# Optimization experiments

Hardware: AMD Instinct MI355X
Metric: run time of the kernel (lower is better)

Reference implementation:

```python
import jax, jax.numpy as jnp
import numpy as np

N_NODES = 50000
N_EDGES = 800000
IN_DIM = 128
E_FEATS = 64
H = 8
D = IN_DIM // H
NEG_SLOPE = 0.2


def setup_inputs() -> dict:
    key = jax.random.key(0)
    ks = jax.random.split(key, 9)
    h = jax.random.normal(ks[0], (N_NODES, IN_DIM), dtype=jnp.float32)
    edge_features = jax.random.normal(ks[1], (N_EDGES, E_FEATS), dtype=jnp.float32)
    src = jax.random.randint(ks[2], (N_EDGES,), 0, N_NODES, dtype=jnp.int32)
    dst = jax.random.randint(ks[3], (N_EDGES,), 0, N_NODES, dtype=jnp.int32)
    s = 0.05
    Wq = jax.random.normal(ks[4], (IN_DIM, IN_DIM), dtype=jnp.float32) * s
    Wk = jax.random.normal(ks[5], (IN_DIM, IN_DIM), dtype=jnp.float32) * s
    Wv = jax.random.normal(ks[6], (IN_DIM, IN_DIM), dtype=jnp.float32) * s
    We = jax.random.normal(ks[7], (H, E_FEATS), dtype=jnp.float32) * s
    Wres = jax.random.normal(ks[8], (IN_DIM, IN_DIM), dtype=jnp.float32) * s
    return {"h": h, "edge_features": edge_features, "src": src, "dst": dst,
            "Wq": Wq, "Wk": Wk, "Wv": Wv, "We": We, "Wres": Wres}


def reference(h, edge_features, src, dst, Wq, Wk, Wv, We, Wres):
    N = h.shape[0]
    # QKV projections (feat_drop is identity at eval)
    q = (h @ Wq.T).reshape(N, H, D)
    k = (h @ Wk.T).reshape(N, H, D)
    v = (h @ Wv.T).reshape(N, H, D)
    # ee / m_att are computed in the original forward but never used (dead code)
    _ee = edge_features @ We.T  # [E, H]

    # v_dot_u('q','k'): dot(q[dst], k[src]) per edge, per head -> [E, H]
    e = jnp.einsum('ehd,ehd->eh', q[dst], k[src])
    e = jnp.where(e >= 0, e, NEG_SLOPE * e)  # leaky_relu

    # edge_softmax over incoming edges of each destination node
    m = jax.ops.segment_max(e, dst, num_segments=N)          # [N, H]
    ex = jnp.exp(e - m[dst])                                 # [E, H]
    z = jax.ops.segment_sum(ex, dst, num_segments=N)         # [N, H]
    alpha = ex / z[dst]                                      # [E, H] (attn_drop identity)

    # weighted aggregation: sum_e alpha * v[src]
    msg = v[src] * alpha[:, :, None]                         # [E, H, D]
    rst = jax.ops.segment_sum(msg, dst, num_segments=N)      # [N, H, D]
    rst = rst.reshape(N, H * D)
    rst = rst + h @ Wres.T                                   # residual
    return rst
```

## Files before the change

### kernel.cpp

```cpp
#include <hip/hip_runtime.h>


#define NEG_SLOPE 0.2f
#define CB 1024

typedef __attribute__((ext_vector_type(8))) short short8;
typedef __attribute__((ext_vector_type(4))) float f32x4;

__device__ __forceinline__ unsigned short f2bf(float f) {
    unsigned int u = __builtin_bit_cast(unsigned int, f);
    u = (u + 0x7fffu + ((u >> 16) & 1u)) >> 16;
    return (unsigned short)u;
}
__device__ __forceinline__ float bf2f(unsigned short s) {
    unsigned int u = (unsigned int)s << 16;
    return __builtin_bit_cast(float, u);
}

__global__ __launch_bounds__(256) void zero_wconv_kernel(
    const float* __restrict__ Wq, const float* __restrict__ Wk,
    const float* __restrict__ Wv, const float* __restrict__ Wres,
    unsigned short* __restrict__ wpk, int* __restrict__ cnt, int n4)
{
    int t = blockIdx.x * 256 + threadIdx.x;
    if (t < 8192) {
        int l = t & 63;
        int v = t >> 6;
        int kk = v & 3;
        int wct = v >> 2;
        int ct = wct & 7;
        int w = wct >> 3;
        const float* W = (w == 0) ? Wq : (w == 1) ? Wk : (w == 2) ? Wv : Wres;
        const float* srcp = W + (size_t)(ct * 16 + (l & 15)) * 128 + kk * 32 + (l >> 4) * 8;
        float4 lo = *reinterpret_cast<const float4*>(srcp);
        float4 hi = *reinterpret_cast<const float4*>(srcp + 4);
        short8 o;
        o[0] = (short)f2bf(lo.x); o[1] = (short)f2bf(lo.y);
        o[2] = (short)f2bf(lo.z); o[3] = (short)f2bf(lo.w);
        o[4] = (short)f2bf(hi.x); o[5] = (short)f2bf(hi.y);
        o[6] = (short)f2bf(hi.z); o[7] = (short)f2bf(hi.w);
        *reinterpret_cast<short8*>(wpk + (size_t)t * 8) = o;
    } else {
        int u = t - 8192;
        if (u < n4) reinterpret_cast<int4*>(cnt)[u] = make_int4(0, 0, 0, 0);
    }
}

__global__ __launch_bounds__(256) void proj_count_kernel(
    const float* __restrict__ h,
    const unsigned short* __restrict__ wpk,
    unsigned short* __restrict__ qb, unsigned short* __restrict__ kvb,
    float* __restrict__ res,
    const int* __restrict__ dst, int* __restrict__ cnt,
    int N, int E, int PB)
{
    if (blockIdx.x >= PB) {
        int start = (blockIdx.x - PB) * 256 + threadIdx.x;
        for (int e = start; e < E; e += CB * 256)
            atomicAdd(&cnt[dst[e]], 1);
        return;
    }

    const int wid = threadIdx.x >> 6;
    const int lane = threadIdx.x & 63;
    const int row0 = blockIdx.x * 128 + wid * 32;
    const int r = lane & 15, g = lane >> 4;

    short8 afrag[2][4];
    #pragma unroll
    for (int grp = 0; grp < 2; ++grp) {
        int arow = row0 + grp * 16 + r;
        if (arow >= N) arow = N - 1;
        const float* hrow = h + (size_t)arow * 128 + g * 8;
        #pragma unroll
        for (int kk = 0; kk < 4; ++kk) {
            float4 lo = *reinterpret_cast<const float4*>(hrow + kk * 32);
            float4 hi = *reinterpret_cast<const float4*>(hrow + kk * 32 + 4);
            short8 a;
            a[0] = (short)f2bf(lo.x); a[1] = (short)f2bf(lo.y);
            a[2] = (short)f2bf(lo.z); a[3] = (short)f2bf(lo.w);
            a[4] = (short)f2bf(hi.x); a[5] = (short)f2bf(hi.y);
            a[6] = (short)f2bf(hi.z); a[7] = (short)f2bf(hi.w);
            afrag[grp][kk] = a;
        }
    }

    for (int w = 0; w < 4; ++w) {
        f32x4 acc[2][8];
        #pragma unroll
        for (int grp = 0; grp < 2; ++grp)
            #pragma unroll
            for (int ct = 0; ct < 8; ++ct) acc[grp][ct] = (f32x4)(0.f);

        #pragma unroll
        for (int ct = 0; ct < 8; ++ct) {
            const unsigned short* bp =
                wpk + ((size_t)((w * 8 + ct) * 4) * 64 + lane) * 8;
            short8 bfrag[4];
            #pragma unroll
            for (int kk = 0; kk < 4; ++kk)
                bfrag[kk] = *reinterpret_cast<const short8*>(bp + (size_t)kk * 512);
            #pragma unroll
            for (int grp = 0; grp < 2; ++grp)
                #pragma unroll
                for (int kk = 0; kk < 4; ++kk)
                    acc[grp][ct] = __builtin_amdgcn_mfma_f32_16x16x32_bf16(
                        afrag[grp][kk], bfrag[kk], acc[grp][ct], 0, 0, 0);
        }

        #pragma unroll
        for (int grp = 0; grp < 2; ++grp) {
            #pragma unroll
            for (int j = 0; j < 4; ++j) {
                int orow = row0 + grp * 16 + g * 4 + j;
                if (orow < N) {
                    if (w == 0) {
                        #pragma unroll
                        for (int ct = 0; ct < 8; ++ct)
                            qb[(size_t)orow * 128 + ct * 16 + r] = f2bf(acc[grp][ct][j]);
                    } else if (w == 3) {
                        #pragma unroll
                        for (int ct = 0; ct < 8; ++ct)
                            res[(size_t)orow * 128 + ct * 16 + r] = acc[grp][ct][j];
                    } else {
                        const int voff = (w == 2) ? 1 : 0;
                        #pragma unroll
                        for (int ct = 0; ct < 8; ++ct) {
                            int idx = ct * 32 + 2 * r + voff;
                            kvb[(size_t)orow * 256 + idx] = f2bf(acc[grp][ct][j]);
                        }
                    }
                }
            }
        }
    }
}

__global__ __launch_bounds__(256) void blocksum_kernel(
    const int* __restrict__ cnt, int* __restrict__ bsum, int N)
{
    __shared__ int ws[4];
    const int tid = threadIdx.x;
    int base = blockIdx.x * 1024 + tid * 4;
    int s = 0;
    if (base + 3 < N) {
        int4 v = *reinterpret_cast<const int4*>(cnt + base);
        s = v.x + v.y + v.z + v.w;
    } else {
        for (int i = 0; i < 4; ++i)
            if (base + i < N) s += cnt[base + i];
    }
    #pragma unroll
    for (int m = 32; m >= 1; m >>= 1) s += __shfl_xor(s, m, 64);
    if ((tid & 63) == 0) ws[tid >> 6] = s;
    __syncthreads();
    if (tid == 0) bsum[blockIdx.x] = ws[0] + ws[1] + ws[2] + ws[3];
}

__global__ __launch_bounds__(256) void scanfinal_kernel(
    const int* __restrict__ cnt, const int* __restrict__ bsum,
    int* __restrict__ row_start, int* __restrict__ cursor,
    int N, int E, int NB)
{
    __shared__ int sboff;
    __shared__ int wsum[4];
    const int tid = threadIdx.x, lane = tid & 63, w = tid >> 6;

    if (tid < 64) {
        int v = (tid < NB && tid < blockIdx.x) ? bsum[tid] : 0;
        #pragma unroll
        for (int m = 32; m >= 1; m >>= 1) v += __shfl_xor(v, m, 64);
        if (tid == 0) sboff = v;
    }
    __syncthreads();

    int base = blockIdx.x * 1024 + tid * 4;
    int a0 = 0, a1 = 0, a2 = 0, a3 = 0;
    if (base + 3 < N) {
        int4 v = *reinterpret_cast<const int4*>(cnt + base);
        a0 = v.x; a1 = v.y; a2 = v.z; a3 = v.w;
    } else {
        if (base + 0 < N) a0 = cnt[base + 0];
        if (base + 1 < N) a1 = cnt[base + 1];
        if (base + 2 < N) a2 = cnt[base + 2];
        if (base + 3 < N) a3 = cnt[base + 3];
    }
    const int tsum = a0 + a1 + a2 + a3;
    int v = tsum;
    #pragma unroll
    for (int off = 1; off < 64; off <<= 1) {
        int t = __shfl_up(v, off, 64);
        if (lane >= off) v += t;
    }
    if (lane == 63) wsum[w] = v;
    __syncthreads();
    int woff = 0;
    for (int i = 0; i < w; ++i) woff += wsum[i];
    int run = sboff + woff + v - tsum;

    int r0 = run, r1 = run + a0, r2 = r1 + a1, r3 = r2 + a2;
    if (base + 3 < N) {
        int4 o = make_int4(r0, r1, r2, r3);
        *reinterpret_cast<int4*>(row_start + base) = o;
        *reinterpret_cast<int4*>(cursor + base) = o;
    } else {
        int rr[4] = {r0, r1, r2, r3};
        for (int i = 0; i < 4; ++i)
            if (base + i < N) { row_start[base + i] = rr[i]; cursor[base + i] = rr[i]; }
    }
    if (blockIdx.x == 0 && tid == 0) row_start[N] = E;
}

__global__ __launch_bounds__(256) void scatter_kernel(
    const int* __restrict__ src, const int* __restrict__ dst,
    int* __restrict__ cursor, int* __restrict__ csr_src, int E)
{
    int e = blockIdx.x * 256 + threadIdx.x;
    if (e < E) {
        int d = dst[e];
        int pos = atomicAdd(&cursor[d], 1);
        csr_src[pos] = src[e];
    }
}

__global__ __launch_bounds__(256) void fused_agg_kernel(
    const unsigned short* __restrict__ qb,
    const unsigned short* __restrict__ kvb,
    const int* __restrict__ row_start, const int* __restrict__ csr_src,
    float* __restrict__ rst, int N)
{
    const int lane = threadIdx.x & 63;
    const int j = lane & 31;
    const int half = lane >> 5;
    const int node = blockIdx.x * 4 + (threadIdx.x >> 6);
    if (node >= N) return;

    const int beg = row_start[node];
    const int nE  = row_start[node + 1] - beg;
    if (nE <= 0) return;
    const int* cp = csr_src + beg;
    const int last = nE - 1;

    ushort4 qraw = *reinterpret_cast<const ushort4*>(qb + (size_t)node * 128 + 4 * j);
    const float q0 = bf2f(qraw.x), q1 = bf2f(qraw.y),
                q2 = bf2f(qraw.z), q3 = bf2f(qraw.w);

    float a0 = 0.f, a1 = 0.f, a2 = 0.f, a3 = 0.f, z = 0.f;

    int sa = cp[min(half, last)];
    int sb = cp[min(half + 2, last)];

    #pragma unroll 2
    for (int i = 0; i < nE; i += 2) {
        const int ii = i + half;
        const float m = (ii < nE) ? 1.f : 0.f;
        const int scur = sa;
        sa = sb;
        sb = cp[min(ii + 4, last)];

        const unsigned short* kp = kvb + (size_t)scur * 256 + 8 * j;
        short8 kv8 = *reinterpret_cast<const short8*>(kp);
        float p = q0 * bf2f((unsigned short)kv8[0])
                + q1 * bf2f((unsigned short)kv8[2])
                + q2 * bf2f((unsigned short)kv8[4])
                + q3 * bf2f((unsigned short)kv8[6]);
        p += __shfl_xor(p, 1, 64);
        p += __shfl_xor(p, 2, 64);
        float e = (p >= 0.f) ? p : NEG_SLOPE * p;
        e = m * __expf(e);
        z += e;
        a0 = fmaf(e, bf2f((unsigned short)kv8[1]), a0);
        a1 = fmaf(e, bf2f((unsigned short)kv8[3]), a1);
        a2 = fmaf(e, bf2f((unsigned short)kv8[5]), a2);
        a3 = fmaf(e, bf2f((unsigned short)kv8[7]), a3);
    }

    a0 += __shfl_xor(a0, 32, 64);
    a1 += __shfl_xor(a1, 32, 64);
    a2 += __shfl_xor(a2, 32, 64);
    a3 += __shfl_xor(a3, 32, 64);
    z  += __shfl_xor(z, 32, 64);

    if (half == 0) {
        const size_t base = (size_t)node * 128 + 4 * j;
        float inv = 1.f / z;
        float4 rv = *reinterpret_cast<const float4*>(rst + base);
        rv.x = fmaf(a0, inv, rv.x);
        rv.y = fmaf(a1, inv, rv.y);
        rv.z = fmaf(a2, inv, rv.z);
        rv.w = fmaf(a3, inv, rv.w);
        *reinterpret_cast<float4*>(rst + base) = rv;
    }
}

extern "C" void kernel_launch(void* const* d_in, const int* in_sizes, int n_in,
                              void* d_out, int out_size, void* d_ws, size_t ws_size,
                              hipStream_t stream) {
    const float* h    = (const float*)d_in[0];
    const int*   src  = (const int*)d_in[2];
    const int*   dst  = (const int*)d_in[3];
    const float* Wq   = (const float*)d_in[4];
    const float* Wk   = (const float*)d_in[5];
    const float* Wv   = (const float*)d_in[6];
    const float* Wres = (const float*)d_in[8];
    float* rst = (float*)d_out;

    const int N = in_sizes[0] / 128;
    const int E = in_sizes[2];

    unsigned short* qb  = (unsigned short*)d_ws;
    unsigned short* kvb = qb + (size_t)N * 128;
    unsigned short* wpk = kvb + (size_t)N * 256;
    int* cnt       = (int*)(wpk + 4 * 16384);
    int* row_start = cnt + N;
    int* cursor    = row_start + (N + 1);
    int* csr_src   = cursor + N;
    int* bsum      = csr_src + E;

    const int n4 = N / 4;
    const int NB = (N + 1023) / 1024;
    const int PB = (N + 127) / 128;

    zero_wconv_kernel<<<(8192 + n4 + 255) / 256, 256, 0, stream>>>(
        Wq, Wk, Wv, Wres, wpk, cnt, n4);
    proj_count_kernel<<<PB + CB, 256, 0, stream>>>(h, wpk, qb, kvb, rst,
                                                   dst, cnt, N, E, PB);
    blocksum_kernel<<<NB, 256, 0, stream>>>(cnt, bsum, N);
    scanfinal_kernel<<<NB, 256, 0, stream>>>(cnt, bsum, row_start, cursor,
                                             N, E, NB);
    scatter_kernel<<<(E + 255) / 256, 256, 0, stream>>>(src, dst, cursor,
                                                        csr_src, E);
    fused_agg_kernel<<<(N + 3) / 4, 256, 0, stream>>>(qb, kvb, row_start,
                                                      csr_src, rst, N);
}
```

Before: 173.8 us.

## Store residual in bf16, pack K/V stores, and unroll aggregation with dual accumulators

The projection kernel now writes the residual projection as bf16 to a workspace buffer instead of fp32 into the output. K and V are computed together per column tile and stored as packed 32-bit words, and accumulator register use drops from 2x8 to per-tile accumulators. The aggregation kernel processes four edges per iteration with two independent accumulator sets to expose more memory-level parallelism. It also reads the bf16 residual and writes the output for zero-degree nodes too. This lowers residual write and read traffic and register pressure, but the residual loses precision by being rounded to bf16.

```diff
diff --git a/kernel.cpp b/kernel.cpp
--- a/kernel.cpp
+++ b/kernel.cpp
@@ -49,8 +49,8 @@
 __global__ __launch_bounds__(256) void proj_count_kernel(
     const float* __restrict__ h,
     const unsigned short* __restrict__ wpk,
-    unsigned short* __restrict__ qb, unsigned short* __restrict__ kvb,
-    float* __restrict__ res,
+    unsigned short* __restrict__ qb, unsigned int* __restrict__ kvb32,
+    unsigned short* __restrict__ resb,
     const int* __restrict__ dst, int* __restrict__ cnt,
     int N, int E, int PB)
 {
@@ -85,54 +85,64 @@
         }
     }
 
-    for (int w = 0; w < 4; ++w) {
-        f32x4 acc[2][8];
-        #pragma unroll
-        for (int grp = 0; grp < 2; ++grp)
-            #pragma unroll
-            for (int ct = 0; ct < 8; ++ct) acc[grp][ct] = (f32x4)(0.f);
-
+    #pragma unroll
+    for (int sec = 0; sec < 2; ++sec) {
+        const int w = (sec == 0) ? 0 : 3;
+        unsigned short* O = (sec == 0) ? qb : resb;
         #pragma unroll
         for (int ct = 0; ct < 8; ++ct) {
             const unsigned short* bp =
                 wpk + ((size_t)((w * 8 + ct) * 4) * 64 + lane) * 8;
-            short8 bfrag[4];
+            f32x4 acc[2];
+            acc[0] = (f32x4)(0.f); acc[1] = (f32x4)(0.f);
             #pragma unroll
-            for (int kk = 0; kk < 4; ++kk)
-                bfrag[kk] = *reinterpret_cast<const short8*>(bp + (size_t)kk * 512);
+            for (int kk = 0; kk < 4; ++kk) {
+                short8 bfrag = *reinterpret_cast<const short8*>(bp + (size_t)kk * 512);
+                acc[0] = __builtin_amdgcn_mfma_f32_16x16x32_bf16(
+                    afrag[0][kk], bfrag, acc[0], 0, 0, 0);
+                acc[1] = __builtin_amdgcn_mfma_f32_16x16x32_bf16(
+                    afrag[1][kk], bfrag, acc[1], 0, 0, 0);
+            }
             #pragma unroll
             for (int grp = 0; grp < 2; ++grp)
                 #pragma unroll
-                for (int kk = 0; kk < 4; ++kk)
-                    acc[grp][ct] = __builtin_amdgcn_mfma_f32_16x16x32_bf16(
-                        afrag[grp][kk], bfrag[kk], acc[grp][ct], 0, 0, 0);
+                for (int j = 0; j < 4; ++j) {
+                    int orow = row0 + grp * 16 + g * 4 + j;
+                    if (orow < N)
+                        O[(size_t)orow * 128 + ct * 16 + r] = f2bf(acc[grp][j]);
+                }
         }
-
-        #pragma unroll
-        for (int grp = 0; grp < 2; ++grp) {
+    }
+
+    #pragma unroll
+    for (int ct = 0; ct < 8; ++ct) {
+        const unsigned short* bp1 =
+            wpk + ((size_t)((1 * 8 + ct) * 4) * 64 + lane) * 8;
+        const unsigned short* bp2 =
+            wpk + ((size_t)((2 * 8 + ct) * 4) * 64 + lane) * 8;
+        f32x4 ak[2], av[2];
+        ak[0] = (f32x4)(0.f); ak[1] = (f32x4)(0.f);
+        av[0] = (f32x4)(0.f); av[1] = (f32x4)(0.f);
+        #pragma unroll
+        for (int kk = 0; kk < 4; ++kk) {
+            short8 b1 = *reinterpret_cast<const short8*>(bp1 + (size_t)kk * 512);
+            short8 b2 = *reinterpret_cast<const short8*>(bp2 + (size_t)kk * 512);
+            ak[0] = __builtin_amdgcn_mfma_f32_16x16x32_bf16(afrag[0][kk], b1, ak[0], 0, 0, 0);
+            ak[1] = __builtin_amdgcn_mfma_f32_16x16x32_bf16(afrag[1][kk], b1, ak[1], 0, 0, 0);
+            av[0] = __builtin_amdgcn_mfma_f32_16x16x32_bf16(afrag[0][kk], b2, av[0], 0, 0, 0);
+            av[1] = __builtin_amdgcn_mfma_f32_16x16x32_bf16(afrag[1][kk], b2, av[1], 0, 0, 0);
+        }
+        #pragma unroll
+        for (int grp = 0; grp < 2; ++grp)
             #pragma unroll
             for (int j = 0; j < 4; ++j) {
                 int orow = row0 + grp * 16 + g * 4 + j;
                 if (orow < N) {
-                    if (w == 0) {
-                        #pragma unroll
-                        for (int ct = 0; ct < 8; ++ct)
-                            qb[(size_t)orow * 128 + ct * 16 + r] = f2bf(acc[grp][ct][j]);
-                    } else if (w == 3) {
-                        #pragma unroll
-                        for (int ct = 0; ct < 8; ++ct)
-                            res[(size_t)orow * 128 + ct * 16 + r] = acc[grp][ct][j];
-                    } else {
-                        const int voff = (w == 2) ? 1 : 0;
-                        #pragma unroll
-                        for (int ct = 0; ct < 8; ++ct) {
-                            int idx = ct * 32 + 2 * r + voff;
-                            kvb[(size_t)orow * 256 + idx] = f2bf(acc[grp][ct][j]);
-                        }
-                    }
+                    unsigned int pk = (unsigned int)f2bf(ak[grp][j])
+                                    | ((unsigned int)f2bf(av[grp][j]) << 16);
+                    kvb32[(size_t)orow * 128 + ct * 16 + r] = pk;
                 }
             }
-        }
     }
 }
 
@@ -226,6 +236,7 @@
 __global__ __launch_bounds__(256) void fused_agg_kernel(
     const unsigned short* __restrict__ qb,
     const unsigned short* __restrict__ kvb,
+    const unsigned short* __restrict__ resb,
     const int* __restrict__ row_start, const int* __restrict__ csr_src,
     float* __restrict__ rst, int N)
 {
@@ -237,44 +248,63 @@
 
     const int beg = row_start[node];
     const int nE  = row_start[node + 1] - beg;
-    if (nE <= 0) return;
     const int* cp = csr_src + beg;
-    const int last = nE - 1;
 
     ushort4 qraw = *reinterpret_cast<const ushort4*>(qb + (size_t)node * 128 + 4 * j);
     const float q0 = bf2f(qraw.x), q1 = bf2f(qraw.y),
                 q2 = bf2f(qraw.z), q3 = bf2f(qraw.w);
 
-    float a0 = 0.f, a1 = 0.f, a2 = 0.f, a3 = 0.f, z = 0.f;
-
-    int sa = cp[min(half, last)];
-    int sb = cp[min(half + 2, last)];
-
-    #pragma unroll 2
-    for (int i = 0; i < nE; i += 2) {
-        const int ii = i + half;
-        const float m = (ii < nE) ? 1.f : 0.f;
-        const int scur = sa;
-        sa = sb;
-        sb = cp[min(ii + 4, last)];
-
-        const unsigned short* kp = kvb + (size_t)scur * 256 + 8 * j;
-        short8 kv8 = *reinterpret_cast<const short8*>(kp);
-        float p = q0 * bf2f((unsigned short)kv8[0])
-                + q1 * bf2f((unsigned short)kv8[2])
-                + q2 * bf2f((unsigned short)kv8[4])
-                + q3 * bf2f((unsigned short)kv8[6]);
-        p += __shfl_xor(p, 1, 64);
-        p += __shfl_xor(p, 2, 64);
-        float e = (p >= 0.f) ? p : NEG_SLOPE * p;
-        e = m * __expf(e);
-        z += e;
-        a0 = fmaf(e, bf2f((unsigned short)kv8[1]), a0);
-        a1 = fmaf(e, bf2f((unsigned short)kv8[3]), a1);
-        a2 = fmaf(e, bf2f((unsigned short)kv8[5]), a2);
-        a3 = fmaf(e, bf2f((unsigned short)kv8[7]), a3);
-    }
-
+    float zA = 0.f, zB = 0.f;
+    float aA0 = 0.f, aA1 = 0.f, aA2 = 0.f, aA3 = 0.f;
+    float aB0 = 0.f, aB1 = 0.f, aB2 = 0.f, aB3 = 0.f;
+
+    if (nE > 0) {
+        const int last = nE - 1;
+        int sa = cp[min(half, last)];
+        int sb = cp[min(half + 2, last)];
+
+        for (int i = 0; i < nE; i += 4) {
+            const int ii = i + half;
+            const float m0 = (ii < nE) ? 1.f : 0.f;
+            const float m1 = (ii + 2 < nE) ? 1.f : 0.f;
+            const int s0 = sa, s1 = sb;
+            sa = cp[min(ii + 4, last)];
+            sb = cp[min(ii + 6, last)];
+
+            short8 kv0 = *reinterpret_cast<const short8*>(kvb + (size_t)s0 * 256 + 8 * j);
+            short8 kv1 = *reinterpret_cast<const short8*>(kvb + (size_t)s1 * 256 + 8 * j);
+
+            float p0 = q0 * bf2f((unsigned short)kv0[0])
+                     + q1 * bf2f((unsigned short)kv0[2])
+                     + q2 * bf2f((unsigned short)kv0[4])
+                     + q3 * bf2f((unsigned short)kv0[6]);
+            float p1 = q0 * bf2f((unsigned short)kv1[0])
+                     + q1 * bf2f((unsigned short)kv1[2])
+                     + q2 * bf2f((unsigned short)kv1[4])
+                     + q3 * bf2f((unsigned short)kv1[6]);
+            p0 += __shfl_xor(p0, 1, 64);
+            p0 += __shfl_xor(p0, 2, 64);
+            p1 += __shfl_xor(p1, 1, 64);
+            p1 += __shfl_xor(p1, 2, 64);
+            float e0 = (p0 >= 0.f) ? p0 : NEG_SLOPE * p0;
+            float e1 = (p1 >= 0.f) ? p1 : NEG_SLOPE * p1;
+            e0 = m0 * __expf(e0);
+            e1 = m1 * __expf(e1);
+            zA += e0;
+            zB += e1;
+            aA0 = fmaf(e0, bf2f((unsigned short)kv0[1]), aA0);
+            aA1 = fmaf(e0, bf2f((unsigned short)kv0[3]), aA1);
+            aA2 = fmaf(e0, bf2f((unsigned short)kv0[5]), aA2);
+            aA3 = fmaf(e0, bf2f((unsigned short)kv0[7]), aA3);
+            aB0 = fmaf(e1, bf2f((unsigned short)kv1[1]), aB0);
+            aB1 = fmaf(e1, bf2f((unsigned short)kv1[3]), aB1);
+            aB2 = fmaf(e1, bf2f((unsigned short)kv1[5]), aB2);
+            aB3 = fmaf(e1, bf2f((unsigned short)kv1[7]), aB3);
+        }
+    }
+
+    float a0 = aA0 + aB0, a1 = aA1 + aB1, a2 = aA2 + aB2, a3 = aA3 + aB3;
+    float z = zA + zB;
     a0 += __shfl_xor(a0, 32, 64);
     a1 += __shfl_xor(a1, 32, 64);
     a2 += __shfl_xor(a2, 32, 64);
@@ -283,12 +313,13 @@
 
     if (half == 0) {
         const size_t base = (size_t)node * 128 + 4 * j;
-        float inv = 1.f / z;
-        float4 rv = *reinterpret_cast<const float4*>(rst + base);
-        rv.x = fmaf(a0, inv, rv.x);
-        rv.y = fmaf(a1, inv, rv.y);
-        rv.z = fmaf(a2, inv, rv.z);
-        rv.w = fmaf(a3, inv, rv.w);
+        ushort4 rb = *reinterpret_cast<const ushort4*>(resb + base);
+        float inv = (nE > 0) ? 1.f / z : 0.f;
+        float4 rv;
+        rv.x = fmaf(a0, inv, bf2f(rb.x));
+        rv.y = fmaf(a1, inv, bf2f(rb.y));
+        rv.z = fmaf(a2, inv, bf2f(rb.z));
+        rv.w = fmaf(a3, inv, bf2f(rb.w));
         *reinterpret_cast<float4*>(rst + base) = rv;
     }
 }
@@ -308,9 +339,10 @@
     const int N = in_sizes[0] / 128;
     const int E = in_sizes[2];
 
-    unsigned short* qb  = (unsigned short*)d_ws;
-    unsigned short* kvb = qb + (size_t)N * 128;
-    unsigned short* wpk = kvb + (size_t)N * 256;
+    unsigned short* qb   = (unsigned short*)d_ws;
+    unsigned short* kvb  = qb + (size_t)N * 128;
+    unsigned short* resb = kvb + (size_t)N * 256;
+    unsigned short* wpk  = resb + (size_t)N * 128;
     int* cnt       = (int*)(wpk + 4 * 16384);
     int* row_start = cnt + N;
     int* cursor    = row_start + (N + 1);
@@ -323,13 +355,14 @@
 
     zero_wconv_kernel<<<(8192 + n4 + 255) / 256, 256, 0, stream>>>(
         Wq, Wk, Wv, Wres, wpk, cnt, n4);
-    proj_count_kernel<<<PB + CB, 256, 0, stream>>>(h, wpk, qb, kvb, rst,
-                                                   dst, cnt, N, E, PB);
+    proj_count_kernel<<<PB + CB, 256, 0, stream>>>(
+        h, wpk, qb, (unsigned int*)kvb, resb, dst, cnt, N, E, PB);
     blocksum_kernel<<<NB, 256, 0, stream>>>(cnt, bsum, N);
     scanfinal_kernel<<<NB, 256, 0, stream>>>(cnt, bsum, row_start, cursor,
                                              N, E, NB);
     scatter_kernel<<<(E + 255) / 256, 256, 0, stream>>>(src, dst, cursor,
                                                         csr_src, E);
-    fused_agg_kernel<<<(N + 3) / 4, 256, 0, stream>>>(qb, kvb, row_start,
-                                                      csr_src, rst, N);
-}
+    fused_agg_kernel<<<(N + 3) / 4, 256, 0, stream>>>(qb, kvb, resb,
+                                                      row_start, csr_src,
+                                                      rst, N);
+}
```

Result: no change. 175.3 us (+0.9%).
